# Performance work log

Hardware: AMD Instinct MI355X
Metric: run time of the kernel (lower is better)

Reference implementation:

```python
import jax, jax.numpy as jnp
import numpy as np

DIM_H = 128
HEADS = 8
HEAD_DIM = DIM_H // HEADS
N_NODES = 40000
N_EDGES = 640000
BN_EPS = 1e-5


def setup_inputs() -> dict:
    key = jax.random.key(0)
    ks = jax.random.split(key, 16)
    s = 0.05
    x = jax.random.normal(ks[0], (N_NODES, DIM_H), dtype=jnp.float32)
    edge_index = jax.random.randint(ks[1], (2, N_EDGES), 0, N_NODES, dtype=jnp.int64)
    p = lambda k, shp: jax.random.normal(k, shp, dtype=jnp.float32) * s
    return {
        "x": x,
        "edge_index": edge_index,
        "Wk": p(ks[2], (DIM_H, DIM_H)), "bk": p(ks[3], (DIM_H,)),
        "Wv": p(ks[4], (DIM_H, DIM_H)), "bv": p(ks[5], (DIM_H,)),
        "Wo": p(ks[6], (DIM_H, DIM_H)), "bo": p(ks[7], (DIM_H,)),
        "bn1_g": jnp.ones((DIM_H,), jnp.float32), "bn1_b": jnp.zeros((DIM_H,), jnp.float32),
        "W1": p(ks[8], (2 * DIM_H, DIM_H)), "b1": p(ks[9], (2 * DIM_H,)),
        "W2": p(ks[10], (DIM_H, 2 * DIM_H)), "b2": p(ks[11], (DIM_H,)),
        "bn2_g": jnp.ones((DIM_H,), jnp.float32), "bn2_b": jnp.zeros((DIM_H,), jnp.float32),
    }


def _batchnorm(h, gamma, beta):
    # BatchNorm1d in training mode: per-feature batch mean / biased var over nodes
    mu = jnp.mean(h, axis=0)
    var = jnp.mean((h - mu) ** 2, axis=0)
    return (h - mu) * jax.lax.rsqrt(var + BN_EPS) * gamma + beta


def _sparse_attn(x, edge_index, Wk, bk, Wv, bv, Wo, bo):
    N = x.shape[0]
    src, dst = edge_index[0], edge_index[1]
    K = (x @ Wk.T + bk).reshape(N, HEADS, HEAD_DIM)
    V = (x @ Wv.T + bv).reshape(N, HEADS, HEAD_DIM)
    Q = x.reshape(N, HEADS, HEAD_DIM)  # query is raw h (no projection)
    # per-edge scores [E, H]
    scores = jnp.sum(K[src] * Q[dst], axis=-1) / np.sqrt(HEAD_DIM).astype(np.float32)
    # segment softmax over destination nodes (pyg_softmax)
    m = jax.ops.segment_max(scores, dst, num_segments=N)
    e = jnp.exp(scores - m[dst])
    denom = jax.ops.segment_sum(e, dst, num_segments=N)
    attn = e / (denom[dst] + 1e-16)  # [E, H]
    messages = V[src] * attn[:, :, None]  # [E, H, D]
    out = jax.ops.segment_sum(messages, dst, num_segments=N)  # [N, H, D]
    return out.reshape(N, DIM_H) @ Wo.T + bo


def reference(x, edge_index, Wk, bk, Wv, bv, Wo, bo, bn1_g, bn1_b,
              W1, b1, W2, b2, bn2_g, bn2_b):
    h_attn = _sparse_attn(x, edge_index, Wk, bk, Wv, bv, Wo, bo)
    h = _batchnorm(x + h_attn, bn1_g, bn1_b)
    ff = jax.nn.relu(h @ W1.T + b1) @ W2.T + b2
    h = _batchnorm(h + ff, bn2_g, bn2_b)
    return h
```

## Files before the change

kernel.cpp:

```cpp
#include <hip/hip_runtime.h>

#define DIM 128
#define NSHARD 8

typedef __attribute__((ext_vector_type(2))) float f32x2;
typedef __attribute__((ext_vector_type(4))) _Float16 half4;
typedef __attribute__((ext_vector_type(8))) _Float16 half8;
typedef __attribute__((ext_vector_type(4))) float f32x4;

#define HP 136
#define UP 264

__device__ __forceinline__ unsigned char to_fp8(float v) {
  return (unsigned char)(__builtin_amdgcn_cvt_pk_fp8_f32(v, v, 0, false) & 0xff);
}

__global__ __launch_bounds__(256) void conv_wall(const float* __restrict__ Wk,
    const float* __restrict__ Wv, const float* __restrict__ Wo,
    const float* __restrict__ W1, const float* __restrict__ W2,
    _Float16* __restrict__ Wkh, _Float16* __restrict__ Wvh,
    _Float16* __restrict__ Woh, _Float16* __restrict__ W1h,
    _Float16* __restrict__ W2h, int* __restrict__ cnt, float* __restrict__ stats,
    int N) {
  int i = blockIdx.x * 256 + threadIdx.x;
  int nth = gridDim.x * 256;
  if (i < 16384) Wkh[i] = (_Float16)Wk[i];
  else if (i < 32768) Wvh[i - 16384] = (_Float16)Wv[i - 16384];
  else if (i < 49152) Woh[i - 32768] = (_Float16)Wo[i - 32768];
  else if (i < 81920) W1h[i - 49152] = (_Float16)W1[i - 49152];
  else if (i < 114688) W2h[i - 81920] = (_Float16)W2[i - 81920];
  for (int j = i; j < N * NSHARD; j += nth) cnt[j] = 0;
  if (i < 512) stats[i] = 0.f;
}

__global__ __launch_bounds__(256) void kv_mfma(const float* __restrict__ x,
    const _Float16* __restrict__ Wkh, const float* __restrict__ bk,
    const _Float16* __restrict__ Wvh, const float* __restrict__ bv,
    unsigned char* __restrict__ KV8, int N) {
  __shared__ _Float16 xs[64 * HP];
  int tid = threadIdx.x;
  int base = blockIdx.x * 64;
  int lane = tid & 63, w = tid >> 6;
  int l15 = lane & 15, quad = lane >> 4;

  for (int i = tid; i < 64 * 32; i += 256) {
    int m = i >> 5, c4 = i & 31;
    float4 tv = ((const float4*)x)[(size_t)(base + m) * 32 + c4];
    half4 hv;
    hv.x = (_Float16)tv.x; hv.y = (_Float16)tv.y;
    hv.z = (_Float16)tv.z; hv.w = (_Float16)tv.w;
    *(half4*)&xs[m * HP + c4 * 4] = hv;
  }
  __syncthreads();

  half8 afr[4][4];
#pragma unroll
  for (int mt = 0; mt < 4; mt++)
#pragma unroll
    for (int ks = 0; ks < 4; ks++)
      afr[mt][ks] = *(const half8*)&xs[(mt * 16 + l15) * HP + ks * 32 + quad * 8];

  const _Float16* W = (w < 2) ? Wkh : Wvh;
  const float* bias = (w < 2) ? bk : bv;
  int voff = (w < 2) ? 0 : 4;
  int c0 = (w & 1) * 64;

#pragma unroll
  for (int nt = 0; nt < 4; nt++) {
    int f = c0 + nt * 16 + l15;
    half8 bfr[4];
#pragma unroll
    for (int ks = 0; ks < 4; ks++)
      bfr[ks] = *(const half8*)&W[(size_t)f * 128 + ks * 32 + quad * 8];
    f32x4 acc[4];
#pragma unroll
    for (int mt = 0; mt < 4; mt++) acc[mt] = (f32x4){0.f, 0.f, 0.f, 0.f};
#pragma unroll
    for (int ks = 0; ks < 4; ks++)
#pragma unroll
      for (int mt = 0; mt < 4; mt++)
        acc[mt] = __builtin_amdgcn_mfma_f32_16x16x32_f16(afr[mt][ks], bfr[ks],
                                                          acc[mt], 0, 0, 0);
    float bb = bias[f];
    int fo = (f >> 2) * 8 + (f & 3) + voff;
#pragma unroll
    for (int mt = 0; mt < 4; mt++)
#pragma unroll
      for (int r = 0; r < 4; r++)
        KV8[(size_t)(base + mt * 16 + quad * 4 + r) * 256 + fo] =
            to_fp8(acc[mt][r] + bb);
  }
}

__global__ __launch_bounds__(256) void hist_rank(const int* __restrict__ ei,
    int* __restrict__ cnt, int* __restrict__ rank, int N, int E) {
  int e = blockIdx.x * 256 + threadIdx.x;
  if (e < E) rank[e] = atomicAdd(&cnt[(e & (NSHARD - 1)) * N + ei[E + e]], 1);
}

__global__ __launch_bounds__(256) void scanA(const int* __restrict__ cnt,
    int* __restrict__ rs, int* __restrict__ bsum, int N) {
  __shared__ int s[256];
  int t = threadIdx.x;
  int i = blockIdx.x * 256 + t;
  int v = 0;
  if (i < N)
#pragma unroll
    for (int sh = 0; sh < NSHARD; sh++) v += cnt[sh * N + i];
  s[t] = v;
  __syncthreads();
  for (int off = 1; off < 256; off <<= 1) {
    int add = (t >= off) ? s[t - off] : 0;
    __syncthreads();
    s[t] += add;
    __syncthreads();
  }
  if (i < N) rs[i] = s[t] - v;
  if (t == 255) bsum[blockIdx.x] = s[t];
}

__global__ __launch_bounds__(256) void scanB(int* __restrict__ bsum, int nb) {
  __shared__ int s[256];
  int t = threadIdx.x;
  int v = (t < nb) ? bsum[t] : 0;
  s[t] = v;
  __syncthreads();
  for (int off = 1; off < 256; off <<= 1) {
    int add = (t >= off) ? s[t - off] : 0;
    __syncthreads();
    s[t] += add;
    __syncthreads();
  }
  if (t < nb) bsum[t] = s[t] - v;
}

__global__ __launch_bounds__(256) void scanC(int* __restrict__ rs,
    const int* __restrict__ bsum, const int* __restrict__ cnt,
    int* __restrict__ rs_shard, int N, int E) {
  int i = blockIdx.x * 256 + threadIdx.x;
  if (i < N) {
    int b = rs[i] + bsum[blockIdx.x];
    rs[i] = b;
#pragma unroll
    for (int sh = 0; sh < NSHARD; sh++) {
      rs_shard[sh * N + i] = b;
      b += cnt[sh * N + i];
    }
  }
  if (i == 0) rs[N] = E;
}

__global__ __launch_bounds__(256) void scatter2(const int* __restrict__ ei,
    const int* __restrict__ rs_shard, const int* __restrict__ rank,
    int* __restrict__ esrc, int N, int E) {
  int e = blockIdx.x * 256 + threadIdx.x;
  if (e < E)
    esrc[rs_shard[(e & (NSHARD - 1)) * N + ei[E + e]] + rank[e]] = ei[e];
}

__global__ __launch_bounds__(256) void attn_agg(const unsigned char* __restrict__ KV8,
    const float* __restrict__ x, const int* __restrict__ rs,
    const int* __restrict__ esrc, _Float16* __restrict__ attn16, int N) {
  int wave = threadIdx.x >> 6, lane = threadIdx.x & 63;
  int n = blockIdx.x * 4 + wave;
  if (n >= N) return;
  int l = lane & 31, s = lane >> 5;
  float4 q = *(const float4*)&x[(size_t)n * DIM + 4 * l];
  int beg = rs[n], end = rs[n + 1];
  float a0 = 0.f, a1 = 0.f, a2 = 0.f, a3 = 0.f, dloc = 0.f;
  for (int e = beg + s; e < end; e += 8) {
    bool hh[4];
    int ss[4];
#pragma unroll
    for (int u = 0; u < 4; u++) hh[u] = (e + 2 * u) < end;
    ss[0] = esrc[e];
#pragma unroll
    for (int u = 1; u < 4; u++) ss[u] = hh[u] ? esrc[e + 2 * u] : ss[0];
    uint2 kv[4];
#pragma unroll
    for (int u = 0; u < 4; u++)
      kv[u] = *(const uint2*)&KV8[(size_t)ss[u] * 256 + 8 * l];
    float p[4];
#pragma unroll
    for (int u = 0; u < 4; u++) {
      f32x2 k01 = __builtin_amdgcn_cvt_pk_f32_fp8(kv[u].x, false);
      f32x2 k23 = __builtin_amdgcn_cvt_pk_f32_fp8(kv[u].x, true);
      p[u] = k01[0] * q.x + k01[1] * q.y + k23[0] * q.z + k23[1] * q.w;
    }
#pragma unroll
    for (int u = 0; u < 4; u++) p[u] += __shfl_xor(p[u], 1);
#pragma unroll
    for (int u = 0; u < 4; u++) p[u] += __shfl_xor(p[u], 2);
#pragma unroll
    for (int u = 0; u < 4; u++) {
      float ev = hh[u] ? __expf(p[u] * 0.25f) : 0.f;
      dloc += ev;
      f32x2 v01 = __builtin_amdgcn_cvt_pk_f32_fp8(kv[u].y, false);
      f32x2 v23 = __builtin_amdgcn_cvt_pk_f32_fp8(kv[u].y, true);
      a0 += ev * v01[0];
      a1 += ev * v01[1];
      a2 += ev * v23[0];
      a3 += ev * v23[1];
    }
  }
  dloc += __shfl_xor(dloc, 32);
  a0 += __shfl_xor(a0, 32);
  a1 += __shfl_xor(a1, 32);
  a2 += __shfl_xor(a2, 32);
  a3 += __shfl_xor(a3, 32);
  if (s == 0) {
    float inv = 1.0f / (dloc + 1e-16f);
    half4 o;
    o.x = (_Float16)(a0 * inv);
    o.y = (_Float16)(a1 * inv);
    o.z = (_Float16)(a2 * inv);
    o.w = (_Float16)(a3 * inv);
    *(half4*)&attn16[(size_t)n * DIM + 4 * l] = o;
  }
}

__global__ __launch_bounds__(256) void o_proj_mfma(const _Float16* __restrict__ attn16,
    const float* __restrict__ x, const _Float16* __restrict__ Woh,
    const float* __restrict__ bo, float* __restrict__ t,
    float* __restrict__ stats, int N) {
  __shared__ _Float16 as16[64 * HP];
  int tid = threadIdx.x;
  int base = blockIdx.x * 64;
  int lane = tid & 63, w = tid >> 6;
  int l15 = lane & 15, quad = lane >> 4;

  for (int i = tid; i < 64 * 16; i += 256) {
    int m = i >> 4, c8 = i & 15;
    *(half8*)&as16[m * HP + c8 * 8] =
        ((const half8*)attn16)[(size_t)(base + m) * 16 + c8];
  }
  __syncthreads();

  half8 afr[4][4];
#pragma unroll
  for (int mt = 0; mt < 4; mt++)
#pragma unroll
    for (int ks = 0; ks < 4; ks++)
      afr[mt][ks] = *(const half8*)&as16[(mt * 16 + l15) * HP + ks * 32 + quad * 8];

  int c0 = w * 32;
  f32x4 acc[4][2];
#pragma unroll
  for (int mt = 0; mt < 4; mt++)
#pragma unroll
    for (int nt = 0; nt < 2; nt++) acc[mt][nt] = (f32x4){0.f, 0.f, 0.f, 0.f};
#pragma unroll
  for (int ks = 0; ks < 4; ks++) {
    half8 b[2];
#pragma unroll
    for (int nt = 0; nt < 2; nt++)
      b[nt] = *(const half8*)&Woh[(size_t)(c0 + nt * 16 + l15) * 128 + ks * 32 +
                                  quad * 8];
#pragma unroll
    for (int mt = 0; mt < 4; mt++)
#pragma unroll
      for (int nt = 0; nt < 2; nt++)
        acc[mt][nt] =
            __builtin_amdgcn_mfma_f32_16x16x32_f16(afr[mt][ks], b[nt], acc[mt][nt], 0, 0, 0);
  }

#pragma unroll
  for (int nt = 0; nt < 2; nt++) {
    int f = c0 + nt * 16 + l15;
    float bb = bo[f];
    float s = 0.f, q = 0.f;
#pragma unroll
    for (int mt = 0; mt < 4; mt++) {
#pragma unroll
      for (int r = 0; r < 4; r++) {
        int row = mt * 16 + quad * 4 + r;
        float tv = acc[mt][nt][r] + bb + x[(size_t)(base + row) * DIM + f];
        t[(size_t)(base + row) * DIM + f] = tv;
        s += tv;
        q += tv * tv;
      }
    }
    s += __shfl_xor(s, 16);
    s += __shfl_xor(s, 32);
    q += __shfl_xor(q, 16);
    q += __shfl_xor(q, 32);
    if (quad == 0) {
      atomicAdd(&stats[f], s);
      atomicAdd(&stats[128 + f], q);
    }
  }
}

__global__ __launch_bounds__(256) void ffn_mfma(const float* __restrict__ t,
    const float* __restrict__ stats1, const float* __restrict__ g1,
    const float* __restrict__ bb1, const _Float16* __restrict__ W1h,
    const float* __restrict__ b1, const _Float16* __restrict__ W2h,
    const float* __restrict__ b2, float* __restrict__ z,
    float* __restrict__ stats2, float invN, int N) {
  __shared__ _Float16 hs[64 * HP];
  __shared__ _Float16 us[64 * UP];
  __shared__ float cf[256];
  int tid = threadIdx.x;
  int base = blockIdx.x * 64;
  int lane = tid & 63, w = tid >> 6;
  int l15 = lane & 15, quad = lane >> 4;

  if (tid < 128) {
    float mu = stats1[tid] * invN;
    float var = stats1[128 + tid] * invN - mu * mu;
    float a = rsqrtf(var + 1e-5f) * g1[tid];
    cf[tid] = a;
    cf[128 + tid] = bb1[tid] - mu * a;
  }
  __syncthreads();

  for (int i = tid; i < 64 * 32; i += 256) {
    int m = i >> 5, c4 = i & 31;
    float4 tv = ((const float4*)t)[(size_t)(base + m) * 32 + c4];
    float4 ca = ((const float4*)cf)[c4];
    float4 cc = ((const float4*)cf)[32 + c4];
    half4 hv;
    hv.x = (_Float16)(tv.x * ca.x + cc.x);
    hv.y = (_Float16)(tv.y * ca.y + cc.y);
    hv.z = (_Float16)(tv.z * ca.z + cc.z);
    hv.w = (_Float16)(tv.w * ca.w + cc.w);
    *(half4*)&hs[m * HP + c4 * 4] = hv;
  }
  __syncthreads();

  int n0 = w * 64;
  half8 afr[4][4];
#pragma unroll
  for (int mt = 0; mt < 4; mt++)
#pragma unroll
    for (int ks = 0; ks < 4; ks++)
      afr[mt][ks] = *(const half8*)&hs[(mt * 16 + l15) * HP + ks * 32 + quad * 8];

#pragma unroll
  for (int nt = 0; nt < 4; nt++) {
    int n = n0 + nt * 16 + l15;
    half8 bfr[4];
#pragma unroll
    for (int ks = 0; ks < 4; ks++)
      bfr[ks] = *(const half8*)&W1h[(size_t)n * 128 + ks * 32 + quad * 8];
    f32x4 acc[4];
#pragma unroll
    for (int mt = 0; mt < 4; mt++) acc[mt] = (f32x4){0.f, 0.f, 0.f, 0.f};
#pragma unroll
    for (int ks = 0; ks < 4; ks++)
#pragma unroll
      for (int mt = 0; mt < 4; mt++)
        acc[mt] = __builtin_amdgcn_mfma_f32_16x16x32_f16(afr[mt][ks], bfr[ks],
                                                          acc[mt], 0, 0, 0);
    float bias = b1[n];
#pragma unroll
    for (int mt = 0; mt < 4; mt++)
#pragma unroll
      for (int r = 0; r < 4; r++)
        us[(mt * 16 + quad * 4 + r) * UP + n] =
            (_Float16)fmaxf(acc[mt][r] + bias, 0.f);
  }
  __syncthreads();

  int n2 = w * 32;
  f32x4 acc2[4][2];
#pragma unroll
  for (int mt = 0; mt < 4; mt++)
#pragma unroll
    for (int nt = 0; nt < 2; nt++) acc2[mt][nt] = (f32x4){0.f, 0.f, 0.f, 0.f};
  for (int ks = 0; ks < 8; ks++) {
    half8 a[4], b[2];
#pragma unroll
    for (int mt = 0; mt < 4; mt++)
      a[mt] = *(const half8*)&us[(mt * 16 + l15) * UP + ks * 32 + quad * 8];
#pragma unroll
    for (int nt = 0; nt < 2; nt++)
      b[nt] = *(const half8*)&W2h[(size_t)(n2 + nt * 16 + l15) * 256 + ks * 32 +
                                  quad * 8];
#pragma unroll
    for (int mt = 0; mt < 4; mt++)
#pragma unroll
      for (int nt = 0; nt < 2; nt++)
        acc2[mt][nt] =
            __builtin_amdgcn_mfma_f32_16x16x32_f16(a[mt], b[nt], acc2[mt][nt], 0, 0, 0);
  }

#pragma unroll
  for (int nt = 0; nt < 2; nt++) {
    int f = n2 + nt * 16 + l15;
    float bz = b2[f];
    float s = 0.f, q = 0.f;
#pragma unroll
    for (int mt = 0; mt < 4; mt++) {
#pragma unroll
      for (int r = 0; r < 4; r++) {
        int row = mt * 16 + quad * 4 + r;
        float hv = (float)hs[row * HP + f];
        float zv = hv + acc2[mt][nt][r] + bz;
        z[(size_t)(base + row) * DIM + f] = zv;
        s += zv;
        q += zv * zv;
      }
    }
    s += __shfl_xor(s, 16);
    s += __shfl_xor(s, 32);
    q += __shfl_xor(q, 16);
    q += __shfl_xor(q, 32);
    if (quad == 0) {
      atomicAdd(&stats2[f], s);
      atomicAdd(&stats2[128 + f], q);
    }
  }
}

__global__ __launch_bounds__(256) void final_apply(const float* __restrict__ z,
    const float* __restrict__ stats2, const float* __restrict__ g2,
    const float* __restrict__ bb2, float* __restrict__ out, float invN,
    int total4) {
  __shared__ float cf[256];
  int tid = threadIdx.x;
  if (tid < 128) {
    float mu = stats2[tid] * invN;
    float var = stats2[128 + tid] * invN - mu * mu;
    float a = rsqrtf(var + 1e-5f) * g2[tid];
    cf[tid] = a;
    cf[128 + tid] = bb2[tid] - mu * a;
  }
  __syncthreads();
  int i = blockIdx.x * 256 + tid;
  if (i >= total4) return;
  int f = (i * 4) & 127;
  float4 zv = ((const float4*)z)[i];
  float4 o;
  o.x = zv.x * cf[f] + cf[128 + f];
  o.y = zv.y * cf[f + 1] + cf[128 + f + 1];
  o.z = zv.z * cf[f + 2] + cf[128 + f + 2];
  o.w = zv.w * cf[f + 3] + cf[128 + f + 3];
  ((float4*)out)[i] = o;
}

extern "C" void kernel_launch(void* const* d_in, const int* in_sizes, int n_in,
                              void* d_out, int out_size, void* d_ws, size_t ws_size,
                              hipStream_t stream) {
  const float* x = (const float*)d_in[0];
  const int* ei = (const int*)d_in[1];
  const float* Wk = (const float*)d_in[2];
  const float* bk = (const float*)d_in[3];
  const float* Wv = (const float*)d_in[4];
  const float* bv = (const float*)d_in[5];
  const float* Wo = (const float*)d_in[6];
  const float* bo = (const float*)d_in[7];
  const float* bn1_g = (const float*)d_in[8];
  const float* bn1_b = (const float*)d_in[9];
  const float* W1 = (const float*)d_in[10];
  const float* b1 = (const float*)d_in[11];
  const float* W2 = (const float*)d_in[12];
  const float* b2 = (const float*)d_in[13];
  const float* bn2_g = (const float*)d_in[14];
  const float* bn2_b = (const float*)d_in[15];
  float* out = (float*)d_out;

  int N = in_sizes[0] / DIM;
  int E = in_sizes[1] / 2;

  unsigned char* KV8 = (unsigned char*)d_ws;
  _Float16* attn16 = (_Float16*)(KV8 + (size_t)N * 256);
  float* zbuf = (float*)(attn16 + (size_t)N * DIM);
  float* tbuf = zbuf + (size_t)N * DIM;
  _Float16* W1h = (_Float16*)(tbuf + (size_t)N * DIM);
  _Float16* W2h = W1h + 32768;
  _Float16* Wkh = W2h + 32768;
  _Float16* Wvh = Wkh + 16384;
  _Float16* Woh = Wvh + 16384;
  float* stats = (float*)(Woh + 16384);
  int* cnt = (int*)(stats + 512);
  int* rs = cnt + (size_t)N * NSHARD;
  int* rs_shard = rs + N + 1;
  int* rank = rs_shard + (size_t)N * NSHARD;
  int* esrc = rank + E;
  int* bsum = esrc + E;

  int nblk = (N + 255) / 256;
  float invN = 1.0f / N;

  conv_wall<<<512, 256, 0, stream>>>(Wk, Wv, Wo, W1, W2, Wkh, Wvh, Woh, W1h, W2h,
                                     cnt, stats, N);
  kv_mfma<<<N / 64, 256, 0, stream>>>(x, Wkh, bk, Wvh, bv, KV8, N);
  hist_rank<<<(E + 255) / 256, 256, 0, stream>>>(ei, cnt, rank, N, E);
  scanA<<<nblk, 256, 0, stream>>>(cnt, rs, bsum, N);
  scanB<<<1, 256, 0, stream>>>(bsum, nblk);
  scanC<<<nblk, 256, 0, stream>>>(rs, bsum, cnt, rs_shard, N, E);
  scatter2<<<(E + 255) / 256, 256, 0, stream>>>(ei, rs_shard, rank, esrc, N, E);
  attn_agg<<<(N + 3) / 4, 256, 0, stream>>>(KV8, x, rs, esrc, attn16, N);
  o_proj_mfma<<<N / 64, 256, 0, stream>>>(attn16, x, Woh, bo, tbuf, stats, N);
  ffn_mfma<<<N / 64, 256, 0, stream>>>(tbuf, stats, bn1_g, bn1_b, W1h, b1, W2h, b2,
                                       zbuf, stats + 256, invN, N);
  final_apply<<<((N * DIM / 4) + 255) / 256, 256, 0, stream>>>(
      zbuf, stats + 256, bn2_g, bn2_b, out, invN, N * DIM / 4);
}
```

Before: 251.3 us.

## Use atomic cursors for CSR scatter and widen attention gather to 16-byte loads

The CSR build no longer stores a per-edge rank array during the histogram. Each edge's slot is claimed later with an atomicAdd on a per-shard cursor during the scatter, which removes one E-sized write and read but makes edge order within a node nondeterministic. The attention aggregation now has each lane load 16 bytes of K/V (8 features) instead of 8. Sixteen edges are processed per iteration across four lane groups, which halves the shuffle reduction per edge but needs more registers and adds cross-group reductions.

```diff
diff --git a/kernel.cpp b/kernel.cpp
--- a/kernel.cpp
+++ b/kernel.cpp
@@ -92,10 +92,10 @@
   }
 }
 
-__global__ __launch_bounds__(256) void hist_rank(const int* __restrict__ ei,
-    int* __restrict__ cnt, int* __restrict__ rank, int N, int E) {
+__global__ __launch_bounds__(256) void hist8(const int* __restrict__ ei,
+    int* __restrict__ cnt, int N, int E) {
   int e = blockIdx.x * 256 + threadIdx.x;
-  if (e < E) rank[e] = atomicAdd(&cnt[(e & (NSHARD - 1)) * N + ei[E + e]], 1);
+  if (e < E) atomicAdd(&cnt[(e & (NSHARD - 1)) * N + ei[E + e]], 1);
 }
 
 __global__ __launch_bounds__(256) void scanA(const int* __restrict__ cnt,
@@ -136,26 +136,27 @@
 
 __global__ __launch_bounds__(256) void scanC(int* __restrict__ rs,
     const int* __restrict__ bsum, const int* __restrict__ cnt,
-    int* __restrict__ rs_shard, int N, int E) {
+    int* __restrict__ cursor, int N, int E) {
   int i = blockIdx.x * 256 + threadIdx.x;
   if (i < N) {
     int b = rs[i] + bsum[blockIdx.x];
     rs[i] = b;
 #pragma unroll
     for (int sh = 0; sh < NSHARD; sh++) {
-      rs_shard[sh * N + i] = b;
+      cursor[sh * N + i] = b;
       b += cnt[sh * N + i];
     }
   }
   if (i == 0) rs[N] = E;
 }
 
-__global__ __launch_bounds__(256) void scatter2(const int* __restrict__ ei,
-    const int* __restrict__ rs_shard, const int* __restrict__ rank,
-    int* __restrict__ esrc, int N, int E) {
+__global__ __launch_bounds__(256) void scatter3(const int* __restrict__ ei,
+    int* __restrict__ cursor, int* __restrict__ esrc, int N, int E) {
   int e = blockIdx.x * 256 + threadIdx.x;
-  if (e < E)
-    esrc[rs_shard[(e & (NSHARD - 1)) * N + ei[E + e]] + rank[e]] = ei[e];
+  if (e < E) {
+    int pos = atomicAdd(&cursor[(e & (NSHARD - 1)) * N + ei[E + e]], 1);
+    esrc[pos] = ei[e];
+  }
 }
 
 __global__ __launch_bounds__(256) void attn_agg(const unsigned char* __restrict__ KV8,
@@ -164,58 +165,69 @@
   int wave = threadIdx.x >> 6, lane = threadIdx.x & 63;
   int n = blockIdx.x * 4 + wave;
   if (n >= N) return;
-  int l = lane & 31, s = lane >> 5;
-  float4 q = *(const float4*)&x[(size_t)n * DIM + 4 * l];
+  int li = lane & 15, g = lane >> 4;
+  float4 qa = *(const float4*)&x[(size_t)n * DIM + 8 * li];
+  float4 qb = *(const float4*)&x[(size_t)n * DIM + 8 * li + 4];
   int beg = rs[n], end = rs[n + 1];
-  float a0 = 0.f, a1 = 0.f, a2 = 0.f, a3 = 0.f, dloc = 0.f;
-  for (int e = beg + s; e < end; e += 8) {
+  float acc[8];
+#pragma unroll
+  for (int i = 0; i < 8; i++) acc[i] = 0.f;
+  float dloc = 0.f;
+  for (int e0 = beg + g; e0 < end; e0 += 16) {
     bool hh[4];
     int ss[4];
 #pragma unroll
-    for (int u = 0; u < 4; u++) hh[u] = (e + 2 * u) < end;
-    ss[0] = esrc[e];
-#pragma unroll
-    for (int u = 1; u < 4; u++) ss[u] = hh[u] ? esrc[e + 2 * u] : ss[0];
-    uint2 kv[4];
+    for (int u = 0; u < 4; u++) hh[u] = (e0 + 4 * u) < end;
+    ss[0] = esrc[e0];
+#pragma unroll
+    for (int u = 1; u < 4; u++) ss[u] = hh[u] ? esrc[e0 + 4 * u] : ss[0];
+    uint4 kv[4];
 #pragma unroll
     for (int u = 0; u < 4; u++)
-      kv[u] = *(const uint2*)&KV8[(size_t)ss[u] * 256 + 8 * l];
+      kv[u] = *(const uint4*)&KV8[(size_t)ss[u] * 256 + 16 * li];
     float p[4];
 #pragma unroll
     for (int u = 0; u < 4; u++) {
       f32x2 k01 = __builtin_amdgcn_cvt_pk_f32_fp8(kv[u].x, false);
       f32x2 k23 = __builtin_amdgcn_cvt_pk_f32_fp8(kv[u].x, true);
-      p[u] = k01[0] * q.x + k01[1] * q.y + k23[0] * q.z + k23[1] * q.w;
+      f32x2 k45 = __builtin_amdgcn_cvt_pk_f32_fp8(kv[u].z, false);
+      f32x2 k67 = __builtin_amdgcn_cvt_pk_f32_fp8(kv[u].z, true);
+      p[u] = k01[0] * qa.x + k01[1] * qa.y + k23[0] * qa.z + k23[1] * qa.w +
+             k45[0] * qb.x + k45[1] * qb.y + k67[0] * qb.z + k67[1] * qb.w;
     }
 #pragma unroll
     for (int u = 0; u < 4; u++) p[u] += __shfl_xor(p[u], 1);
-#pragma unroll
-    for (int u = 0; u < 4; u++) p[u] += __shfl_xor(p[u], 2);
 #pragma unroll
     for (int u = 0; u < 4; u++) {
       float ev = hh[u] ? __expf(p[u] * 0.25f) : 0.f;
       dloc += ev;
       f32x2 v01 = __builtin_amdgcn_cvt_pk_f32_fp8(kv[u].y, false);
       f32x2 v23 = __builtin_amdgcn_cvt_pk_f32_fp8(kv[u].y, true);
-      a0 += ev * v01[0];
-      a1 += ev * v01[1];
-      a2 += ev * v23[0];
-      a3 += ev * v23[1];
-    }
-  }
+      f32x2 v45 = __builtin_amdgcn_cvt_pk_f32_fp8(kv[u].w, false);
+      f32x2 v67 = __builtin_amdgcn_cvt_pk_f32_fp8(kv[u].w, true);
+      acc[0] += ev * v01[0];
+      acc[1] += ev * v01[1];
+      acc[2] += ev * v23[0];
+      acc[3] += ev * v23[1];
+      acc[4] += ev * v45[0];
+      acc[5] += ev * v45[1];
+      acc[6] += ev * v67[0];
+      acc[7] += ev * v67[1];
+    }
+  }
+  dloc += __shfl_xor(dloc, 16);
   dloc += __shfl_xor(dloc, 32);
-  a0 += __shfl_xor(a0, 32);
-  a1 += __shfl_xor(a1, 32);
-  a2 += __shfl_xor(a2, 32);
-  a3 += __shfl_xor(a3, 32);
-  if (s == 0) {
+#pragma unroll
+  for (int i = 0; i < 8; i++) {
+    acc[i] += __shfl_xor(acc[i], 16);
+    acc[i] += __shfl_xor(acc[i], 32);
+  }
+  if (g == 0) {
     float inv = 1.0f / (dloc + 1e-16f);
-    half4 o;
-    o.x = (_Float16)(a0 * inv);
-    o.y = (_Float16)(a1 * inv);
-    o.z = (_Float16)(a2 * inv);
-    o.w = (_Float16)(a3 * inv);
-    *(half4*)&attn16[(size_t)n * DIM + 4 * l] = o;
+    half8 o;
+#pragma unroll
+    for (int i = 0; i < 8; i++) o[i] = (_Float16)(acc[i] * inv);
+    *(half8*)&attn16[(size_t)n * DIM + 8 * li] = o;
   }
 }
 
@@ -475,9 +487,8 @@
   float* stats = (float*)(Woh + 16384);
   int* cnt = (int*)(stats + 512);
   int* rs = cnt + (size_t)N * NSHARD;
-  int* rs_shard = rs + N + 1;
-  int* rank = rs_shard + (size_t)N * NSHARD;
-  int* esrc = rank + E;
+  int* cursor = rs + N + 1;
+  int* esrc = cursor + (size_t)N * NSHARD;
   int* bsum = esrc + E;
 
   int nblk = (N + 255) / 256;
@@ -486,11 +497,11 @@
   conv_wall<<<512, 256, 0, stream>>>(Wk, Wv, Wo, W1, W2, Wkh, Wvh, Woh, W1h, W2h,
                                      cnt, stats, N);
   kv_mfma<<<N / 64, 256, 0, stream>>>(x, Wkh, bk, Wvh, bv, KV8, N);
-  hist_rank<<<(E + 255) / 256, 256, 0, stream>>>(ei, cnt, rank, N, E);
+  hist8<<<(E + 255) / 256, 256, 0, stream>>>(ei, cnt, N, E);
   scanA<<<nblk, 256, 0, stream>>>(cnt, rs, bsum, N);
   scanB<<<1, 256, 0, stream>>>(bsum, nblk);
-  scanC<<<nblk, 256, 0, stream>>>(rs, bsum, cnt, rs_shard, N, E);
-  scatter2<<<(E + 255) / 256, 256, 0, stream>>>(ei, rs_shard, rank, esrc, N, E);
+  scanC<<<nblk, 256, 0, stream>>>(rs, bsum, cnt, cursor, N, E);
+  scatter3<<<(E + 255) / 256, 256, 0, stream>>>(ei, cursor, esrc, N, E);
   attn_agg<<<(N + 3) / 4, 256, 0, stream>>>(KV8, x, rs, esrc, attn16, N);
   o_proj_mfma<<<N / 64, 256, 0, stream>>>(attn16, x, Woh, bo, tbuf, stats, N);
   ffn_mfma<<<N / 64, 256, 0, stream>>>(tbuf, stats, bn1_g, bn1_b, W1h, b1, W2h, b2,
```

Result: slower. 278.6 us (+10.9%).
